# Performance work log

Measured on AMD Instinct MI355X. Metric: run time of the kernel, lower is better.

## Reference

```python
import jax, jax.numpy as jnp
import numpy as np
from jax import lax

H = 1024
W = 1024
WIN = 32
STR = 16
NH = (H - WIN) // STR + 1  # 63
N = NH * NH                # 3969 patches
DN3 = ('NCDHW', 'OIDHW', 'NCDHW')
DN2 = ('NCHW', 'OIHW', 'NCHW')


def setup_inputs() -> dict:
    key = jax.random.key(0)
    ks = jax.random.split(key, 13)
    r = lambda k, s, sc=0.05: jax.random.normal(k, s, dtype=jnp.float32) * sc
    return {
        'x1': jax.random.normal(ks[0], (1, 1, 1, H, W), jnp.float32),
        'x2': jax.random.normal(ks[1], (1, 1, 1, H, W), jnp.float32),
        'conv1_w': r(ks[2], (24, 1, 2, 8, 8)),      # Conv3d(1,24,(2,8,8)) [O,I,D,H,W]
        'conv1_b': r(ks[3], (24,)),
        'conv2_w': r(ks[4], (60, 24, 5, 5)),         # Conv2d(24,60,5)
        'conv2_b': r(ks[5], (60,)),
        'deconv2_w': r(ks[6], (60, 24, 5, 5)),       # ConvTranspose2d(60,24,5) [I,O,kH,kW]
        'deconv2_b': r(ks[7], (24,)),
        'deconv1_w': r(ks[8], (24, 1, 2, 8, 8)),     # ConvTranspose3d(24,1,(2,8,8)) [I,O,D,H,W]
        'deconv1_b': r(ks[9], (1,)),
        'lin_w': r(ks[10], (N, 2), 0.5),             # per-patch Linear(2,1) weights
        'lin_b': r(ks[11], (N,), 0.5),               # per-patch Linear(2,1) bias
        'linear1_w': r(ks[12], (1, 1), 0.5),         # Linear(1,1,bias=False)
    }


def _conv(x, w, b, dn):
    nd = w.ndim - 2
    y = lax.conv_general_dilated(x, w, (1,) * nd, 'VALID', dimension_numbers=dn)
    return y + b.reshape((1, -1) + (1,) * nd)


def _convT(x, w, b, dn):
    # stride-1, pad-0 transposed conv == full-pad conv with flipped, IO-swapped kernel
    nd = w.ndim - 2
    wf = jnp.flip(w, axis=tuple(range(2, w.ndim))).swapaxes(0, 1)  # [O,I,*k]
    pad = [(k - 1, k - 1) for k in w.shape[2:]]
    y = lax.conv_general_dilated(x, wf, (1,) * nd, pad, dimension_numbers=dn)
    return y + b.reshape((1, -1) + (1,) * nd)


def reference(x1, x2, conv1_w, conv1_b, conv2_w, conv2_b, deconv2_w, deconv2_b,
              deconv1_w, deconv1_b, lin_w, lin_b, linear1_w):
    x = jnp.concatenate([x1, x2], axis=2)[0, 0]  # [2,H,W]
    idx = (jnp.arange(NH) * STR)[:, None] + jnp.arange(WIN)[None, :]  # [NH,32]
    # unfold dims 3,4 with window 32 / stride 16 -> [2,NH,NW,32,32]
    patches = x[:, idx[:, None, :, None], idx[None, :, None, :]]
    outX = patches.reshape(2, N, WIN, WIN).transpose(1, 0, 2, 3)[:, None]  # [N,1,2,32,32]
    h = jax.nn.elu(_conv(outX, conv1_w, conv1_b, DN3))        # [N,24,1,25,25]
    h = jax.nn.relu(_conv(h[:, :, 0], conv2_w, conv2_b, DN2))  # [N,60,21,21]
    h = jax.nn.elu(_convT(h, deconv2_w, deconv2_b, DN2))       # [N,24,25,25]
    h = _convT(h[:, :, None], deconv1_w, deconv1_b, DN3)       # [N,1,2,32,32]
    # per-patch Linear(2,1) over depth channels, batched over all patches
    p = jnp.einsum('nchw,nc->nhw', h[:, 0], lin_w) + lin_b[:, None, None]  # [N,32,32]
    p = p.reshape(NH, NH, WIN, WIN)
    # col2im: overlap-add fold, block 32, stride 16 -> [H,W]
    recon = jnp.zeros((H, W), jnp.float32).at[idx[:, None, :, None], idx[None, :, None, :]].add(p)
    outX2 = recon * linear1_w[0, 0]  # Linear(1,1,bias=False) per pixel
    return x2 - outX2.reshape(x2.shape)
```

## Files before the change

### kernel.cpp

```cpp
#include <hip/hip_runtime.h>
#include <hip/hip_bf16.h>

static constexpr int H_ = 1024;
static constexpr int W_ = 1024;
static constexpr int STR_ = 16;
static constexpr int NH_ = 63;
static constexpr int NPATCH_ = NH_ * NH_;

typedef short bf16x8 __attribute__((ext_vector_type(8)));
typedef short short4v __attribute__((ext_vector_type(4)));
typedef float f32x4 __attribute__((ext_vector_type(4)));

static constexpr int SH1_STRIDE = 72;
static constexpr int SH2_BASE   = 45056;
static constexpr int SH2_STRIDE = 80;
static constexpr int ZROW_REL   = 441 * SH2_STRIDE;
static constexpr int SPB0       = 45056;
static constexpr int SPB1       = 50176;
static constexpr int H3_STRIDE  = 80;
static constexpr int SWC_BASE   = 51200;
static constexpr int SP_ACC     = 56320;
static constexpr int LDS_BYTES  = 80416;

__device__ __forceinline__ unsigned short f2bf(float x) {
    __hip_bfloat16 b = __float2bfloat16(x);
    return __builtin_bit_cast(unsigned short, b);
}

__global__ __launch_bounds__(512, 2) void fused_patch_kernel(
    const float* __restrict__ x1, const float* __restrict__ x2,
    const float* __restrict__ c1b, const float* __restrict__ c2b,
    const float* __restrict__ d2b, const float* __restrict__ d1b,
    const float* __restrict__ lin_w, const float* __restrict__ lin_b,
    const unsigned short* __restrict__ w1frag,
    const unsigned short* __restrict__ w2frag,
    const unsigned short* __restrict__ dw2frag,
    const float* __restrict__ dw1,
    float* __restrict__ recon)
{
    __shared__ alignas(16) char sbuf[LDS_BYTES];
    const int n  = blockIdx.x;
    const int t  = (int)threadIdx.x;
    const int pi = n / NH_, pj = n % NH_;
    const int Y0 = pi * STR_, X0 = pj * STR_;
    const int wv = t >> 6, lane = t & 63;
    const int ln15 = lane & 15, quad = lane >> 4;

    if (t < 20) ((float*)(sbuf + SH2_BASE + ZROW_REL))[t] = 0.f;
    for (int k = t; k < 2048; k += 512) {
        int d = k >> 10, r = k & 1023, y = r >> 5, x = r & 31;
        unsigned short b = f2bf((d ? x2 : x1)[(Y0 + y) * W_ + (X0 + x)]);
        int row = (d * 32 + y) * 40;
        ((unsigned short*)(sbuf + SPB0))[row + x] = b;
        if (x > 0) ((unsigned short*)(sbuf + SPB1))[row + x - 1] = b;
    }
    __syncthreads();

    {
        bf16x8 bw[4][2];
        #pragma unroll
        for (int kc = 0; kc < 4; ++kc)
            #pragma unroll
            for (int nt = 0; nt < 2; ++nt)
                bw[kc][nt] = *(const bf16x8*)(w1frag + (((kc * 2 + nt) * 64) + lane) * 8);

        for (int tl = wv; tl < 50; tl += 8) {
            const int vcol = tl >> 1, ubase = (tl & 1) * 16;
            const int u = ubase + ln15;
            const char* abase = sbuf + ((vcol & 1) ? SPB1 : SPB0) + (vcol & ~1) * 2;
            f32x4 acc[2];
            acc[0] = (f32x4){0.f, 0.f, 0.f, 0.f};
            acc[1] = (f32x4){0.f, 0.f, 0.f, 0.f};
            #pragma unroll
            for (int kc = 0; kc < 4; ++kc) {
                const int idx8 = kc * 4 + quad;
                const int dd = idx8 >> 3, pp = idx8 & 7;
                const unsigned int* ap = (const unsigned int*)(abase + (dd * 32 + u + pp) * 80);
                union { unsigned int u4[4]; bf16x8 v; } af;
                af.u4[0] = ap[0]; af.u4[1] = ap[1]; af.u4[2] = ap[2]; af.u4[3] = ap[3];
                acc[0] = __builtin_amdgcn_mfma_f32_16x16x32_bf16(af.v, bw[kc][0], acc[0], 0, 0, 0);
                acc[1] = __builtin_amdgcn_mfma_f32_16x16x32_bf16(af.v, bw[kc][1], acc[1], 0, 0, 0);
            }
            #pragma unroll
            for (int ntp = 0; ntp < 2; ++ntp) {
                const int c = ntp * 16 + ln15;
                const float bias = (c < 24) ? c1b[c] : 0.f;
                #pragma unroll
                for (int r = 0; r < 4; ++r) {
                    int uu = ubase + quad * 4 + r;
                    if (uu < 25) {
                        float hv = acc[ntp][r] + bias;
                        hv = hv > 0.f ? hv : expm1f(hv);
                        *(unsigned short*)(sbuf + (uu * 25 + vcol) * SH1_STRIDE + c * 2) = f2bf(hv);
                    }
                }
            }
        }
    }
    __syncthreads();

    f32x4 acc3[5][2];
    {
        f32x4 z4 = {0.f, 0.f, 0.f, 0.f};
        #pragma unroll
        for (int i = 0; i < 5; ++i) { acc3[i][0] = z4; acc3[i][1] = z4; }
    }

    #pragma unroll
    for (int kc = 0; kc < 2; ++kc) {
        if (wv < 7) {
            const int mt0 = wv * 4;
            int abase[4];
            #pragma unroll
            for (int i = 0; i < 4; ++i) {
                int m = (mt0 + i) * 16 + ln15;
                if (m > 440) m = 440;
                abase[i] = ((m / 21) * 25 + (m % 21)) * SH1_STRIDE;
            }
            const int o0 = kc * 32 + ln15, o1 = o0 + 16;
            const float bias0 = c2b[o0];
            const float bias1 = (o1 < 60) ? c2b[o1] : 0.f;

            f32x4 z4 = {0.f, 0.f, 0.f, 0.f};
            f32x4 acc2[4][2];
            #pragma unroll
            for (int i = 0; i < 4; ++i) { acc2[i][0] = z4; acc2[i][1] = z4; }

            const unsigned short* wb = w2frag + lane * 8;
            #pragma unroll
            for (int p = 0; p < 5; ++p) {
                #pragma unroll
                for (int q = 0; q < 5; ++q) {
                    const int tap  = p * 5 + q;
                    const int toff = (p * 25 + q) * SH1_STRIDE;
                    bf16x8 b0 = *(const bf16x8*)(wb + (tap * 4 + kc * 2 + 0) * 512);
                    bf16x8 b1 = *(const bf16x8*)(wb + (tap * 4 + kc * 2 + 1) * 512);
                    #pragma unroll
                    for (int i = 0; i < 4; ++i) {
                        const char* ap = sbuf + abase[i] + toff + quad * 16;
                        short4v lo = *(const short4v*)ap;
                        short4v hi = *(const short4v*)(ap + 8);
                        bf16x8 a = __builtin_shufflevector(lo, hi, 0, 1, 2, 3, 4, 5, 6, 7);
                        acc2[i][0] = __builtin_amdgcn_mfma_f32_16x16x32_bf16(a, b0, acc2[i][0], 0, 0, 0);
                        acc2[i][1] = __builtin_amdgcn_mfma_f32_16x16x32_bf16(a, b1, acc2[i][1], 0, 0, 0);
                    }
                }
            }
            #pragma unroll
            for (int i = 0; i < 4; ++i) {
                #pragma unroll
                for (int r = 0; r < 4; ++r) {
                    int pix = (mt0 + i) * 16 + quad * 4 + r;
                    if (pix < 441) {
                        unsigned short* rowp = (unsigned short*)(sbuf + SH2_BASE + pix * SH2_STRIDE);
                        rowp[ln15]      = f2bf(fmaxf(acc2[i][0][r] + bias0, 0.f));
                        rowp[16 + ln15] = f2bf(fmaxf(acc2[i][1][r] + bias1, 0.f));
                    }
                }
            }
        }
        __syncthreads();

        {
            int uarr[5], varr[5], a80[5];
            bool mval[5];
            #pragma unroll
            for (int i = 0; i < 5; ++i) {
                int m = (wv * 5 + i) * 16 + ln15;
                mval[i] = (m < 625);
                int mc = mval[i] ? m : 0;
                uarr[i] = mc / 25; varr[i] = mc % 25;
                a80[i] = (uarr[i] * 21 + varr[i]) * SH2_STRIDE;
            }
            const unsigned short* db = dw2frag + kc * 1024 + lane * 8;
            #pragma unroll
            for (int dy = 0; dy < 5; ++dy) {
                #pragma unroll
                for (int dx = 0; dx < 5; ++dx) {
                    const int tap   = dy * 5 + dx;
                    const int t2off = (dy * 21 + dx) * SH2_STRIDE;
                    bf16x8 b0 = *(const bf16x8*)(db + tap * 2048);
                    bf16x8 b1 = *(const bf16x8*)(db + tap * 2048 + 512);
                    #pragma unroll
                    for (int i = 0; i < 5; ++i) {
                        int yv = uarr[i] - dy, xv = varr[i] - dx;
                        bool ok = mval[i] && ((unsigned)yv < 21u) && ((unsigned)xv < 21u);
                        int ra = ok ? (a80[i] - t2off) : ZROW_REL;
                        const char* ap = sbuf + SH2_BASE + ra + quad * 16;
                        bf16x8 a = *(const bf16x8*)ap;
                        acc3[i][0] = __builtin_amdgcn_mfma_f32_16x16x32_bf16(a, b0, acc3[i][0], 0, 0, 0);
                        acc3[i][1] = __builtin_amdgcn_mfma_f32_16x16x32_bf16(a, b1, acc3[i][1], 0, 0, 0);
                    }
                }
            }
        }
        __syncthreads();
    }

    const float lw0 = lin_w[2 * n], lw1 = lin_w[2 * n + 1];
    float* sp = (float*)(sbuf + SP_ACC);
    {
        const int c0 = ln15, c1 = 16 + ln15;
        const float db0 = d2b[c0];
        const float db1 = (c1 < 24) ? d2b[c1] : 0.f;
        #pragma unroll
        for (int i = 0; i < 5; ++i) {
            #pragma unroll
            for (int r = 0; r < 4; ++r) {
                int pix = (wv * 5 + i) * 16 + quad * 4 + r;
                if (pix < 625) {
                    float hv = acc3[i][0][r] + db0;
                    hv = hv > 0.f ? hv : expm1f(hv);
                    float hw = acc3[i][1][r] + db1;
                    hw = hw > 0.f ? hw : expm1f(hw);
                    unsigned short* rowp = (unsigned short*)(sbuf + pix * H3_STRIDE);
                    rowp[c0] = f2bf(hv);
                    rowp[c1] = f2bf(hw);
                }
            }
        }
    }
    for (int k = t; k < 2048; k += 512) {
        int r = k >> 5, c = k & 31;
        float v = 0.f;
        if (c < 24)
            v = lw0 * dw1[(c * 2 + 0) * 64 + r] + lw1 * dw1[(c * 2 + 1) * 64 + r];
        ((unsigned short*)(sbuf + SWC_BASE))[r * 40 + c] = f2bf(v);
    }
    for (int k = t; k < 1024; k += 512) sp[k] = 0.f;
    __syncthreads();

    #pragma unroll
    for (int pass = 0; pass < 2; ++pass) {
        bf16x8 wb0 = *(const bf16x8*)(sbuf + SWC_BASE + ((pass * 2 + 0) * 16 + ln15) * 80 + quad * 16);
        bf16x8 wb1 = *(const bf16x8*)(sbuf + SWC_BASE + ((pass * 2 + 1) * 16 + ln15) * 80 + quad * 16);
        f32x4 acc4[5][2];
        {
            f32x4 z4 = {0.f, 0.f, 0.f, 0.f};
            #pragma unroll
            for (int i = 0; i < 5; ++i) { acc4[i][0] = z4; acc4[i][1] = z4; }
        }
        #pragma unroll
        for (int i = 0; i < 5; ++i) {
            int m = (wv * 5 + i) * 16 + ln15;
            if (m > 624) m = 624;
            bf16x8 a = *(const bf16x8*)(sbuf + m * H3_STRIDE + quad * 16);
            acc4[i][0] = __builtin_amdgcn_mfma_f32_16x16x32_bf16(a, wb0, acc4[i][0], 0, 0, 0);
            acc4[i][1] = __builtin_amdgcn_mfma_f32_16x16x32_bf16(a, wb1, acc4[i][1], 0, 0, 0);
        }
        #pragma unroll
        for (int i = 0; i < 5; ++i) {
            #pragma unroll
            for (int r = 0; r < 4; ++r) {
                int pix = (wv * 5 + i) * 16 + quad * 4 + r;
                if (pix < 625) {
                    int u = pix / 25, v = pix % 25;
                    #pragma unroll
                    for (int ntp = 0; ntp < 2; ++ntp) {
                        int rv = (pass * 2 + ntp) * 16 + ln15;
                        atomicAdd(&sp[(u + (rv >> 3)) * 32 + v + (rv & 7)], acc4[i][ntp][r]);
                    }
                }
            }
        }
    }
    __syncthreads();

    const float obias = d1b[0] * (lw0 + lw1) + lin_b[n];
    for (int k = t; k < 1024; k += 512) {
        int yy = k >> 5, xx = k & 31;
        atomicAdd(&recon[(Y0 + yy) * W_ + (X0 + xx)], sp[k] + obias);
    }
}

__global__ void prep_kernel(const float* __restrict__ c1w,
                            const float* __restrict__ c2w,
                            const float* __restrict__ d2w,
                            unsigned short* __restrict__ w1frag,
                            unsigned short* __restrict__ w2frag,
                            unsigned short* __restrict__ dw2frag)
{
    int i = blockIdx.x * blockDim.x + threadIdx.x;
    if (i < 51200) {
        int j = i & 7, lane = (i >> 3) & 63;
        int ln15 = lane & 15, quad = lane >> 4;
        if (i < 4096) {
            int g = i >> 9;
            int kc = g >> 1, nt = g & 1;
            int nn = nt * 16 + ln15, k = kc * 32 + quad * 8 + j;
            w1frag[i] = f2bf((nn < 24) ? c1w[nn * 128 + k] : 0.f);
        }
        {
            int nt = (i >> 9) & 3, tap = i >> 11;
            int o = nt * 16 + ln15, c = quad * 8 + j;
            float v = (o < 60 && c < 24) ? c2w[(o * 24 + c) * 25 + tap] : 0.f;
            w2frag[i] = f2bf(v);
        }
        {
            int nt = (i >> 9) & 1, kc = (i >> 10) & 1, tap = i >> 11;
            int k = kc * 32 + quad * 8 + j, c = nt * 16 + ln15;
            float v = (k < 60 && c < 24) ? d2w[(k * 24 + c) * 25 + tap] : 0.f;
            dw2frag[i] = f2bf(v);
        }
    }
}

__global__ void finalize_kernel(const float* __restrict__ x2,
                                const float* __restrict__ l1w,
                                float* __restrict__ out)
{
    int i = blockIdx.x * blockDim.x + threadIdx.x;
    if (i < H_ * W_) {
        float r = out[i];
        out[i] = x2[i] - r * l1w[0];
    }
}

extern "C" void kernel_launch(void* const* d_in, const int* in_sizes, int n_in,
                              void* d_out, int out_size, void* d_ws, size_t ws_size,
                              hipStream_t stream)
{
    const float* x1  = (const float*)d_in[0];
    const float* x2  = (const float*)d_in[1];
    const float* c1w = (const float*)d_in[2];
    const float* c1b = (const float*)d_in[3];
    const float* c2w = (const float*)d_in[4];
    const float* c2b = (const float*)d_in[5];
    const float* d2w = (const float*)d_in[6];
    const float* d2b = (const float*)d_in[7];
    const float* d1w = (const float*)d_in[8];
    const float* d1b = (const float*)d_in[9];
    const float* lw  = (const float*)d_in[10];
    const float* lb  = (const float*)d_in[11];
    const float* l1w = (const float*)d_in[12];

    float*          out     = (float*)d_out;
    unsigned short* w1frag  = (unsigned short*)d_ws;
    unsigned short* w2frag  = (unsigned short*)((char*)d_ws + 8192);
    unsigned short* dw2frag = (unsigned short*)((char*)d_ws + 110592);

    hipMemsetAsync(d_out, 0, (size_t)H_ * W_ * sizeof(float), stream);
    prep_kernel<<<100, 512, 0, stream>>>(c1w, c2w, d2w, w1frag, w2frag, dw2frag);
    fused_patch_kernel<<<NPATCH_, 512, 0, stream>>>(x1, x2, c1b, c2b, d2b, d1b,
                                                    lw, lb, w1frag, w2frag, dw2frag,
                                                    d1w, out);
    finalize_kernel<<<(H_ * W_ + 255) / 256, 256, 0, stream>>>(x2, l1w, out);
}
```

Baseline: 1.528 ms.

## Double block size to 1024 threads and fuse conv2/deconv2 channel halves

Moves the fused per-patch kernel from 512 to 1024 threads per block. Conv2 now computes all 60 output channels in a single pass, and its full 64-channel output is stored in LDS at once, so deconv2 runs in one pass with two k-chunks instead of two passes separated by barriers. The LDS layout is repacked with smaller strides so the larger buffer fits, and conv1 weight fragments are reloaded from global memory per tile instead of being held in registers. This removes the extra sync and pass overhead and spreads the MFMA work over more waves. The trade-offs are higher LDS per block (about 83KB, which limits blocks per CU), tighter register limits from the 1024-thread launch bound, and idle waves in stages with uneven tile counts.

```diff
diff --git a/kernel.cpp b/kernel.cpp
--- a/kernel.cpp
+++ b/kernel.cpp
@@ -11,23 +11,26 @@
 typedef short short4v __attribute__((ext_vector_type(4)));
 typedef float f32x4 __attribute__((ext_vector_type(4)));
 
-static constexpr int SH1_STRIDE = 72;
-static constexpr int SH2_BASE   = 45056;
-static constexpr int SH2_STRIDE = 80;
+static constexpr int SH1_STRIDE = 48;
+static constexpr int SH2_BASE   = 30016;
+static constexpr int SH2_STRIDE = 120;
 static constexpr int ZROW_REL   = 441 * SH2_STRIDE;
-static constexpr int SPB0       = 45056;
-static constexpr int SPB1       = 50176;
-static constexpr int H3_STRIDE  = 80;
-static constexpr int SWC_BASE   = 51200;
-static constexpr int SP_ACC     = 56320;
-static constexpr int LDS_BYTES  = 80416;
+static constexpr int SPB0       = 30016;
+static constexpr int SPB1       = 35136;
+static constexpr int SWC_BASE   = 30016;
+static constexpr int SP_ACC     = 34112;
+static constexpr int LDS_BYTES  = 83072;
 
 __device__ __forceinline__ unsigned short f2bf(float x) {
     __hip_bfloat16 b = __float2bfloat16(x);
     return __builtin_bit_cast(unsigned short, b);
 }
 
-__global__ __launch_bounds__(512, 2) void fused_patch_kernel(
+__device__ __forceinline__ f32x4 mfma_bf16(bf16x8 a, bf16x8 b, f32x4 c) {
+    return __builtin_amdgcn_mfma_f32_16x16x32_bf16(a, b, c, 0, 0, 0);
+}
+
+__global__ __launch_bounds__(1024, 4) void fused_patch_kernel(
     const float* __restrict__ x1, const float* __restrict__ x2,
     const float* __restrict__ c1b, const float* __restrict__ c2b,
     const float* __restrict__ d2b, const float* __restrict__ d1b,
@@ -46,8 +49,8 @@
     const int wv = t >> 6, lane = t & 63;
     const int ln15 = lane & 15, quad = lane >> 4;
 
-    if (t < 20) ((float*)(sbuf + SH2_BASE + ZROW_REL))[t] = 0.f;
-    for (int k = t; k < 2048; k += 512) {
+    if (t < 30) ((float*)(sbuf + SH2_BASE + ZROW_REL))[t] = 0.f;
+    for (int k = t; k < 2048; k += 1024) {
         int d = k >> 10, r = k & 1023, y = r >> 5, x = r & 31;
         unsigned short b = f2bf((d ? x2 : x1)[(Y0 + y) * W_ + (X0 + x)]);
         int row = (d * 32 + y) * 40;
@@ -56,35 +59,30 @@
     }
     __syncthreads();
 
-    {
-        bf16x8 bw[4][2];
-        #pragma unroll
-        for (int kc = 0; kc < 4; ++kc)
-            #pragma unroll
-            for (int nt = 0; nt < 2; ++nt)
-                bw[kc][nt] = *(const bf16x8*)(w1frag + (((kc * 2 + nt) * 64) + lane) * 8);
-
-        for (int tl = wv; tl < 50; tl += 8) {
-            const int vcol = tl >> 1, ubase = (tl & 1) * 16;
-            const int u = ubase + ln15;
-            const char* abase = sbuf + ((vcol & 1) ? SPB1 : SPB0) + (vcol & ~1) * 2;
-            f32x4 acc[2];
-            acc[0] = (f32x4){0.f, 0.f, 0.f, 0.f};
-            acc[1] = (f32x4){0.f, 0.f, 0.f, 0.f};
-            #pragma unroll
-            for (int kc = 0; kc < 4; ++kc) {
-                const int idx8 = kc * 4 + quad;
-                const int dd = idx8 >> 3, pp = idx8 & 7;
-                const unsigned int* ap = (const unsigned int*)(abase + (dd * 32 + u + pp) * 80);
-                union { unsigned int u4[4]; bf16x8 v; } af;
-                af.u4[0] = ap[0]; af.u4[1] = ap[1]; af.u4[2] = ap[2]; af.u4[3] = ap[3];
-                acc[0] = __builtin_amdgcn_mfma_f32_16x16x32_bf16(af.v, bw[kc][0], acc[0], 0, 0, 0);
-                acc[1] = __builtin_amdgcn_mfma_f32_16x16x32_bf16(af.v, bw[kc][1], acc[1], 0, 0, 0);
-            }
-            #pragma unroll
-            for (int ntp = 0; ntp < 2; ++ntp) {
-                const int c = ntp * 16 + ln15;
-                const float bias = (c < 24) ? c1b[c] : 0.f;
+    for (int tl = wv; tl < 50; tl += 16) {
+        const int vcol = tl >> 1, ubase = (tl & 1) * 16;
+        const int u = ubase + ln15;
+        const char* abase = sbuf + ((vcol & 1) ? SPB1 : SPB0) + (vcol & ~1) * 2;
+        f32x4 acc[2];
+        acc[0] = (f32x4){0.f, 0.f, 0.f, 0.f};
+        acc[1] = (f32x4){0.f, 0.f, 0.f, 0.f};
+        #pragma unroll
+        for (int kc = 0; kc < 4; ++kc) {
+            const int idx8 = kc * 4 + quad;
+            const int dd = idx8 >> 3, pp = idx8 & 7;
+            const unsigned int* ap = (const unsigned int*)(abase + (dd * 32 + u + pp) * 80);
+            union { unsigned int u4[4]; bf16x8 v; } af;
+            af.u4[0] = ap[0]; af.u4[1] = ap[1]; af.u4[2] = ap[2]; af.u4[3] = ap[3];
+            bf16x8 b0 = *(const bf16x8*)(w1frag + (((kc * 2 + 0) * 64) + lane) * 8);
+            bf16x8 b1 = *(const bf16x8*)(w1frag + (((kc * 2 + 1) * 64) + lane) * 8);
+            acc[0] = mfma_bf16(af.v, b0, acc[0]);
+            acc[1] = mfma_bf16(af.v, b1, acc[1]);
+        }
+        #pragma unroll
+        for (int ntp = 0; ntp < 2; ++ntp) {
+            const int c = ntp * 16 + ln15;
+            if (c < 24) {
+                const float bias = c1b[c];
                 #pragma unroll
                 for (int r = 0; r < 4; ++r) {
                     int uu = ubase + quad * 4 + r;
@@ -99,103 +97,116 @@
     }
     __syncthreads();
 
-    f32x4 acc3[5][2];
+    if (wv < 14) {
+        int abase2[2];
+        #pragma unroll
+        for (int i = 0; i < 2; ++i) {
+            int m = (wv + i * 14) * 16 + ln15;
+            if (m > 440) m = 440;
+            abase2[i] = ((m / 21) * 25 + (m % 21)) * SH1_STRIDE;
+        }
+        float bias[4];
+        #pragma unroll
+        for (int nt = 0; nt < 4; ++nt) {
+            int o = nt * 16 + ln15;
+            bias[nt] = (o < 60) ? c2b[o] : 0.f;
+        }
+        f32x4 acc2[2][4];
+        #pragma unroll
+        for (int i = 0; i < 2; ++i)
+            #pragma unroll
+            for (int nt = 0; nt < 4; ++nt)
+                acc2[i][nt] = (f32x4){0.f, 0.f, 0.f, 0.f};
+
+        const unsigned short* wb = w2frag + lane * 8;
+        #pragma unroll
+        for (int p = 0; p < 5; ++p) {
+            #pragma unroll
+            for (int q = 0; q < 5; ++q) {
+                const int tap  = p * 5 + q;
+                const int toff = (p * 25 + q) * SH1_STRIDE;
+                bf16x8 b[4];
+                #pragma unroll
+                for (int nt = 0; nt < 4; ++nt)
+                    b[nt] = *(const bf16x8*)(wb + (tap * 4 + nt) * 512);
+                #pragma unroll
+                for (int i = 0; i < 2; ++i) {
+                    bf16x8 a = *(const bf16x8*)(sbuf + abase2[i] + toff + quad * 16);
+                    #pragma unroll
+                    for (int nt = 0; nt < 4; ++nt)
+                        acc2[i][nt] = mfma_bf16(a, b[nt], acc2[i][nt]);
+                }
+            }
+        }
+        #pragma unroll
+        for (int i = 0; i < 2; ++i) {
+            #pragma unroll
+            for (int r = 0; r < 4; ++r) {
+                int pix = (wv + i * 14) * 16 + quad * 4 + r;
+                if (pix < 441) {
+                    unsigned short* rowp = (unsigned short*)(sbuf + SH2_BASE + pix * SH2_STRIDE);
+                    #pragma unroll
+                    for (int nt = 0; nt < 4; ++nt) {
+                        int o = nt * 16 + ln15;
+                        if (o < 60)
+                            rowp[o] = f2bf(fmaxf(acc2[i][nt][r] + bias[nt], 0.f));
+                    }
+                }
+            }
+        }
+    }
+    __syncthreads();
+
+    f32x4 acc3[3][2];
     {
-        f32x4 z4 = {0.f, 0.f, 0.f, 0.f};
-        #pragma unroll
-        for (int i = 0; i < 5; ++i) { acc3[i][0] = z4; acc3[i][1] = z4; }
-    }
-
-    #pragma unroll
-    for (int kc = 0; kc < 2; ++kc) {
-        if (wv < 7) {
-            const int mt0 = wv * 4;
-            int abase[4];
-            #pragma unroll
-            for (int i = 0; i < 4; ++i) {
-                int m = (mt0 + i) * 16 + ln15;
-                if (m > 440) m = 440;
-                abase[i] = ((m / 21) * 25 + (m % 21)) * SH1_STRIDE;
-            }
-            const int o0 = kc * 32 + ln15, o1 = o0 + 16;
-            const float bias0 = c2b[o0];
-            const float bias1 = (o1 < 60) ? c2b[o1] : 0.f;
-
-            f32x4 z4 = {0.f, 0.f, 0.f, 0.f};
-            f32x4 acc2[4][2];
-            #pragma unroll
-            for (int i = 0; i < 4; ++i) { acc2[i][0] = z4; acc2[i][1] = z4; }
-
-            const unsigned short* wb = w2frag + lane * 8;
-            #pragma unroll
-            for (int p = 0; p < 5; ++p) {
-                #pragma unroll
-                for (int q = 0; q < 5; ++q) {
-                    const int tap  = p * 5 + q;
-                    const int toff = (p * 25 + q) * SH1_STRIDE;
-                    bf16x8 b0 = *(const bf16x8*)(wb + (tap * 4 + kc * 2 + 0) * 512);
-                    bf16x8 b1 = *(const bf16x8*)(wb + (tap * 4 + kc * 2 + 1) * 512);
-                    #pragma unroll
-                    for (int i = 0; i < 4; ++i) {
-                        const char* ap = sbuf + abase[i] + toff + quad * 16;
-                        short4v lo = *(const short4v*)ap;
-                        short4v hi = *(const short4v*)(ap + 8);
-                        bf16x8 a = __builtin_shufflevector(lo, hi, 0, 1, 2, 3, 4, 5, 6, 7);
-                        acc2[i][0] = __builtin_amdgcn_mfma_f32_16x16x32_bf16(a, b0, acc2[i][0], 0, 0, 0);
-                        acc2[i][1] = __builtin_amdgcn_mfma_f32_16x16x32_bf16(a, b1, acc2[i][1], 0, 0, 0);
-                    }
-                }
-            }
-            #pragma unroll
-            for (int i = 0; i < 4; ++i) {
-                #pragma unroll
-                for (int r = 0; r < 4; ++r) {
-                    int pix = (mt0 + i) * 16 + quad * 4 + r;
-                    if (pix < 441) {
-                        unsigned short* rowp = (unsigned short*)(sbuf + SH2_BASE + pix * SH2_STRIDE);
-                        rowp[ln15]      = f2bf(fmaxf(acc2[i][0][r] + bias0, 0.f));
-                        rowp[16 + ln15] = f2bf(fmaxf(acc2[i][1][r] + bias1, 0.f));
-                    }
-                }
-            }
-        }
-        __syncthreads();
-
-        {
-            int uarr[5], varr[5], a80[5];
-            bool mval[5];
-            #pragma unroll
-            for (int i = 0; i < 5; ++i) {
-                int m = (wv * 5 + i) * 16 + ln15;
-                mval[i] = (m < 625);
-                int mc = mval[i] ? m : 0;
-                uarr[i] = mc / 25; varr[i] = mc % 25;
-                a80[i] = (uarr[i] * 21 + varr[i]) * SH2_STRIDE;
-            }
-            const unsigned short* db = dw2frag + kc * 1024 + lane * 8;
-            #pragma unroll
-            for (int dy = 0; dy < 5; ++dy) {
-                #pragma unroll
-                for (int dx = 0; dx < 5; ++dx) {
-                    const int tap   = dy * 5 + dx;
-                    const int t2off = (dy * 21 + dx) * SH2_STRIDE;
-                    bf16x8 b0 = *(const bf16x8*)(db + tap * 2048);
-                    bf16x8 b1 = *(const bf16x8*)(db + tap * 2048 + 512);
-                    #pragma unroll
-                    for (int i = 0; i < 5; ++i) {
-                        int yv = uarr[i] - dy, xv = varr[i] - dx;
-                        bool ok = mval[i] && ((unsigned)yv < 21u) && ((unsigned)xv < 21u);
-                        int ra = ok ? (a80[i] - t2off) : ZROW_REL;
-                        const char* ap = sbuf + SH2_BASE + ra + quad * 16;
-                        bf16x8 a = *(const bf16x8*)ap;
-                        acc3[i][0] = __builtin_amdgcn_mfma_f32_16x16x32_bf16(a, b0, acc3[i][0], 0, 0, 0);
-                        acc3[i][1] = __builtin_amdgcn_mfma_f32_16x16x32_bf16(a, b1, acc3[i][1], 0, 0, 0);
-                    }
-                }
-            }
-        }
-        __syncthreads();
-    }
+        #pragma unroll
+        for (int i = 0; i < 3; ++i) {
+            acc3[i][0] = (f32x4){0.f, 0.f, 0.f, 0.f};
+            acc3[i][1] = (f32x4){0.f, 0.f, 0.f, 0.f};
+        }
+        int uarr[3], varr[3], a120[3];
+        bool mval[3];
+        #pragma unroll
+        for (int i = 0; i < 3; ++i) {
+            int m = (wv + i * 16) * 16 + ln15;
+            mval[i] = (m < 625);
+            int mc = mval[i] ? m : 0;
+            uarr[i] = mc / 25; varr[i] = mc % 25;
+            a120[i] = (uarr[i] * 21 + varr[i]) * SH2_STRIDE;
+        }
+        const unsigned short* db = dw2frag + lane * 8;
+        #pragma unroll
+        for (int dy = 0; dy < 5; ++dy) {
+            #pragma unroll
+            for (int dx = 0; dx < 5; ++dx) {
+                const int tap   = dy * 5 + dx;
+                const int t2off = (dy * 21 + dx) * SH2_STRIDE;
+                bf16x8 b00 = *(const bf16x8*)(db + tap * 2048);
+                bf16x8 b01 = *(const bf16x8*)(db + tap * 2048 + 512);
+                bf16x8 b10 = *(const bf16x8*)(db + tap * 2048 + 1024);
+                bf16x8 b11 = *(const bf16x8*)(db + tap * 2048 + 1536);
+                #pragma unroll
+                for (int i = 0; i < 3; ++i) {
+                    if (i == 2 && wv >= 8) continue;
+                    int yv = uarr[i] - dy, xv = varr[i] - dx;
+                    bool ok = mval[i] && ((unsigned)yv < 21u) && ((unsigned)xv < 21u);
+                    int ra = ok ? (a120[i] - t2off) : ZROW_REL;
+                    const char* ap = sbuf + SH2_BASE + ra + quad * 16;
+                    short4v lo0 = *(const short4v*)(ap);
+                    short4v hi0 = *(const short4v*)(ap + 8);
+                    bf16x8 a0 = __builtin_shufflevector(lo0, hi0, 0, 1, 2, 3, 4, 5, 6, 7);
+                    acc3[i][0] = mfma_bf16(a0, b00, acc3[i][0]);
+                    acc3[i][1] = mfma_bf16(a0, b01, acc3[i][1]);
+                    short4v lo1 = *(const short4v*)(ap + 64);
+                    short4v hi1 = *(const short4v*)(ap + 72);
+                    bf16x8 a1 = __builtin_shufflevector(lo1, hi1, 0, 1, 2, 3, 4, 5, 6, 7);
+                    acc3[i][0] = mfma_bf16(a1, b10, acc3[i][0]);
+                    acc3[i][1] = mfma_bf16(a1, b11, acc3[i][1]);
+                }
+            }
+        }
+    }
+    __syncthreads();
 
     const float lw0 = lin_w[2 * n], lw1 = lin_w[2 * n + 1];
     float* sp = (float*)(sbuf + SP_ACC);
@@ -204,61 +215,56 @@
         const float db0 = d2b[c0];
         const float db1 = (c1 < 24) ? d2b[c1] : 0.f;
         #pragma unroll
-        for (int i = 0; i < 5; ++i) {
+        for (int i = 0; i < 3; ++i) {
+            if (i == 2 && wv >= 8) continue;
             #pragma unroll
             for (int r = 0; r < 4; ++r) {
-                int pix = (wv * 5 + i) * 16 + quad * 4 + r;
+                int pix = (wv + i * 16) * 16 + quad * 4 + r;
                 if (pix < 625) {
+                    unsigned short* rowp = (unsigned short*)(sbuf + pix * SH1_STRIDE);
                     float hv = acc3[i][0][r] + db0;
-                    hv = hv > 0.f ? hv : expm1f(hv);
-                    float hw = acc3[i][1][r] + db1;
-                    hw = hw > 0.f ? hw : expm1f(hw);
-                    unsigned short* rowp = (unsigned short*)(sbuf + pix * H3_STRIDE);
-                    rowp[c0] = f2bf(hv);
-                    rowp[c1] = f2bf(hw);
-                }
-            }
-        }
-    }
-    for (int k = t; k < 2048; k += 512) {
+                    rowp[c0] = f2bf(hv > 0.f ? hv : expm1f(hv));
+                    if (c1 < 24) {
+                        float hw = acc3[i][1][r] + db1;
+                        rowp[c1] = f2bf(hw > 0.f ? hw : expm1f(hw));
+                    }
+                }
+            }
+        }
+    }
+    for (int k = t; k < 2048; k += 1024) {
         int r = k >> 5, c = k & 31;
         float v = 0.f;
         if (c < 24)
             v = lw0 * dw1[(c * 2 + 0) * 64 + r] + lw1 * dw1[(c * 2 + 1) * 64 + r];
-        ((unsigned short*)(sbuf + SWC_BASE))[r * 40 + c] = f2bf(v);
-    }
-    for (int k = t; k < 1024; k += 512) sp[k] = 0.f;
-    __syncthreads();
-
-    #pragma unroll
-    for (int pass = 0; pass < 2; ++pass) {
-        bf16x8 wb0 = *(const bf16x8*)(sbuf + SWC_BASE + ((pass * 2 + 0) * 16 + ln15) * 80 + quad * 16);
-        bf16x8 wb1 = *(const bf16x8*)(sbuf + SWC_BASE + ((pass * 2 + 1) * 16 + ln15) * 80 + quad * 16);
-        f32x4 acc4[5][2];
-        {
-            f32x4 z4 = {0.f, 0.f, 0.f, 0.f};
-            #pragma unroll
-            for (int i = 0; i < 5; ++i) { acc4[i][0] = z4; acc4[i][1] = z4; }
-        }
-        #pragma unroll
-        for (int i = 0; i < 5; ++i) {
-            int m = (wv * 5 + i) * 16 + ln15;
+        ((unsigned short*)(sbuf + SWC_BASE))[r * 32 + c] = f2bf(v);
+    }
+    sp[t] = 0.f;
+    __syncthreads();
+
+    {
+        bf16x8 wbv[4];
+        #pragma unroll
+        for (int nt = 0; nt < 4; ++nt)
+            wbv[nt] = *(const bf16x8*)(sbuf + SWC_BASE + (nt * 16 + ln15) * 64 + quad * 16);
+        #pragma unroll
+        for (int i = 0; i < 3; ++i) {
+            int mt = wv + i * 16;
+            if (mt >= 40) continue;
+            int m = mt * 16 + ln15;
             if (m > 624) m = 624;
-            bf16x8 a = *(const bf16x8*)(sbuf + m * H3_STRIDE + quad * 16);
-            acc4[i][0] = __builtin_amdgcn_mfma_f32_16x16x32_bf16(a, wb0, acc4[i][0], 0, 0, 0);
-            acc4[i][1] = __builtin_amdgcn_mfma_f32_16x16x32_bf16(a, wb1, acc4[i][1], 0, 0, 0);
-        }
-        #pragma unroll
-        for (int i = 0; i < 5; ++i) {
-            #pragma unroll
-            for (int r = 0; r < 4; ++r) {
-                int pix = (wv * 5 + i) * 16 + quad * 4 + r;
-                if (pix < 625) {
-                    int u = pix / 25, v = pix % 25;
-                    #pragma unroll
-                    for (int ntp = 0; ntp < 2; ++ntp) {
-                        int rv = (pass * 2 + ntp) * 16 + ln15;
-                        atomicAdd(&sp[(u + (rv >> 3)) * 32 + v + (rv & 7)], acc4[i][ntp][r]);
+            bf16x8 a = *(const bf16x8*)(sbuf + m * SH1_STRIDE + quad * 16);
+            #pragma unroll
+            for (int nt = 0; nt < 4; ++nt) {
+                f32x4 acc4 = (f32x4){0.f, 0.f, 0.f, 0.f};
+                acc4 = mfma_bf16(a, wbv[nt], acc4);
+                #pragma unroll
+                for (int r = 0; r < 4; ++r) {
+                    int pix = mt * 16 + quad * 4 + r;
+                    if (pix < 625) {
+                        int u = pix / 25, v = pix % 25;
+                        int rv = nt * 16 + ln15;
+                        atomicAdd(&sp[(u + (rv >> 3)) * 32 + v + (rv & 7)], acc4[r]);
                     }
                 }
             }
@@ -267,9 +273,9 @@
     __syncthreads();
 
     const float obias = d1b[0] * (lw0 + lw1) + lin_b[n];
-    for (int k = t; k < 1024; k += 512) {
-        int yy = k >> 5, xx = k & 31;
-        atomicAdd(&recon[(Y0 + yy) * W_ + (X0 + xx)], sp[k] + obias);
+    {
+        int yy = t >> 5, xx = t & 31;
+        atomicAdd(&recon[(Y0 + yy) * W_ + (X0 + xx)], sp[t] + obias);
     }
 }
 
@@ -341,8 +347,8 @@
 
     hipMemsetAsync(d_out, 0, (size_t)H_ * W_ * sizeof(float), stream);
     prep_kernel<<<100, 512, 0, stream>>>(c1w, c2w, d2w, w1frag, w2frag, dw2frag);
-    fused_patch_kernel<<<NPATCH_, 512, 0, stream>>>(x1, x2, c1b, c2b, d2b, d1b,
-                                                    lw, lb, w1frag, w2frag, dw2frag,
-                                                    d1w, out);
+    fused_patch_kernel<<<NPATCH_, 1024, 0, stream>>>(x1, x2, c1b, c2b, d2b, d1b,
+                                                     lw, lb, w1frag, w2frag, dw2frag,
+                                                     d1w, out);
     finalize_kernel<<<(H_ * W_ + 255) / 256, 256, 0, stream>>>(x2, l1w, out);
 }
```

After: 1.435 ms. 6.1% less time.
